# Optimization experiments

Hardware: AMD Instinct MI355X
Metric: run time of the kernel (lower is better)

The kernel has to match this reference:

```python
import jax, jax.numpy as jnp
import numpy as np
from math import sqrt

B, S, E, H = 4, 2048, 1024, 16
DH = E // H  # 64


def setup_inputs() -> dict:
    key = jax.random.key(0)
    ks = jax.random.split(key, 10)
    sc = 0.02
    return {
        "x": jax.random.normal(ks[0], (B, S, E), dtype=jnp.float32),
        # per-head projection weights stacked: [H, E, DH], biases [H, DH]
        "Wq": jax.random.normal(ks[1], (H, E, DH), dtype=jnp.float32) * sc,
        "bq": jax.random.normal(ks[2], (H, DH), dtype=jnp.float32) * sc,
        "Wk": jax.random.normal(ks[3], (H, E, DH), dtype=jnp.float32) * sc,
        "bk": jax.random.normal(ks[4], (H, DH), dtype=jnp.float32) * sc,
        "Wv": jax.random.normal(ks[5], (H, E, DH), dtype=jnp.float32) * sc,
        "bv": jax.random.normal(ks[6], (H, DH), dtype=jnp.float32) * sc,
        "Wo": jax.random.normal(ks[7], (E, E), dtype=jnp.float32) * sc,
        "bo": jax.random.normal(ks[8], (E,), dtype=jnp.float32) * sc,
    }


def reference(x, Wq, bq, Wk, bk, Wv, bv, Wo, bo):
    # Batched QKV projections (equivalent to the per-head Linear loop)
    q = jnp.einsum("bse,hed->bhsd", x, Wq) + bq[None, :, None, :]
    k = jnp.einsum("bse,hed->bhsd", x, Wk) + bk[None, :, None, :]
    v = jnp.einsum("bse,hed->bhsd", x, Wv) + bv[None, :, None, :]
    scores = jnp.einsum("bhsd,bhtd->bhst", q, k) / sqrt(DH)
    # masked=False in the module, so plain softmax over keys
    weights = jax.nn.softmax(scores, axis=-1)
    attn = jnp.einsum("bhst,bhtd->bhsd", weights, v)
    # concat heads: [B,S,H*DH] with head i contiguous (matches torch.cat dim=-1)
    concat = attn.transpose(0, 2, 1, 3).reshape(B, S, H * DH)
    out = concat @ Wo.T if Wo.shape == (E, E) and False else jnp.einsum("bsf,ef->bse", concat, Wo) + bo
    return out
```

## Files before the change

kernel.cpp:

```cpp
#include <hip/hip_runtime.h>
#include <math.h>

#define Bc 4
#define Sc 2048
#define Ec 1024
#define Hc 16
#define DHc 64

typedef unsigned short u16;
typedef __attribute__((ext_vector_type(8))) short short8;
typedef __attribute__((ext_vector_type(4))) float f32x4;
typedef __attribute__((ext_vector_type(16))) float f32x16;
typedef __attribute__((ext_vector_type(2))) unsigned short u16x2;

union pk8 { unsigned int u[4]; short8 v; };

__device__ __forceinline__ u16 f2bf(float f) {
    unsigned int u = __float_as_uint(f);
    u += 0x7FFFu + ((u >> 16) & 1u);
    return (u16)(u >> 16);
}

__device__ __forceinline__ void gl_lds16(const void* g, void* l) {
    __builtin_amdgcn_global_load_lds(
        (const __attribute__((address_space(1))) unsigned int*)g,
        (__attribute__((address_space(3))) unsigned int*)l,
        16, 0, 0);
}

__global__ __launch_bounds__(256)
void prep_kernel(const float* __restrict__ x,
                 const float* __restrict__ Wq, const float* __restrict__ Wk,
                 const float* __restrict__ Wv, const float* __restrict__ Wo,
                 u16* __restrict__ xb, u16* __restrict__ Wob, u16* __restrict__ Wtb)
{
    __shared__ float T[64][65];
    const int bid = blockIdx.x;
    const int t = threadIdx.x;

    if (bid < 4096 + 512) {
        const float* src = (bid < 4096) ? x : Wo;
        u16* dst = (bid < 4096) ? xb : Wob;
        size_t i = (size_t)(bid < 4096 ? bid : bid - 4096) * 256 + t;
        const float* p = src + i * 8;
        float4 a = *(const float4*)p;
        float4 b = *(const float4*)(p + 4);
        short8 v;
        v[0] = (short)f2bf(a.x); v[1] = (short)f2bf(a.y);
        v[2] = (short)f2bf(a.z); v[3] = (short)f2bf(a.w);
        v[4] = (short)f2bf(b.x); v[5] = (short)f2bf(b.y);
        v[6] = (short)f2bf(b.z); v[7] = (short)f2bf(b.w);
        *(short8*)(dst + i * 8) = v;
        return;
    }

    const int bid2 = bid - 4608;
    const int proj = bid2 >> 8;
    const int h = (bid2 >> 4) & 15;
    const int e0 = (bid2 & 15) * 64;
    const float* W = (proj == 0) ? Wq : (proj == 1) ? Wk : Wv;

    #pragma unroll
    for (int i = 0; i < 4; ++i) {
        int fid = t + i * 256;
        int row = fid >> 4, c4 = fid & 15;
        float4 v = *(const float4*)(W + ((size_t)h * Ec + e0 + row) * DHc + c4 * 4);
        T[row][c4 * 4 + 0] = v.x; T[row][c4 * 4 + 1] = v.y;
        T[row][c4 * 4 + 2] = v.z; T[row][c4 * 4 + 3] = v.w;
    }
    __syncthreads();
    const int d = t >> 2, ech = (t & 3) * 16;
    u16* dst = Wtb + ((size_t)(proj * Hc + h) * DHc + d) * Ec + e0 + ech;
    #pragma unroll
    for (int j = 0; j < 16; j += 2) {
        u16x2 v2;
        v2.x = f2bf(T[ech + j][d]);
        v2.y = f2bf(T[ech + j + 1][d]);
        *(u16x2*)(dst + j) = v2;
    }
}

__global__ __launch_bounds__(256)
void qkv_mfma_kernel(const u16* __restrict__ xb, const u16* __restrict__ Wtb,
                     const float* __restrict__ bq, const float* __restrict__ bk,
                     const float* __restrict__ bv,
                     u16* __restrict__ qb, u16* __restrict__ kb, u16* __restrict__ vb)
{
    __shared__ __align__(16) u16 As[128 * 64];
    __shared__ __align__(16) u16 Bs[128 * 64];

    const int t = threadIdx.x;
    const int w = t >> 6, l = t & 63;
    const int wr = w >> 1, wc = w & 1;
    const int mBase = blockIdx.y * 128;
    const int nBase = blockIdx.x * 128;
    const int proj = nBase >> 10;
    const int nIn = nBase & (Ec - 1);
    const int lr = l >> 3, ls = l & 7;
    const int lq = l >> 4, ln = l & 15;

    f32x4 acc[4][4];
    #pragma unroll
    for (int i = 0; i < 4; ++i)
        #pragma unroll
        for (int j = 0; j < 4; ++j) acc[i][j] = (f32x4)0.f;

    for (int k0 = 0; k0 < Ec; k0 += 64) {
        __syncthreads();
        #pragma unroll
        for (int c = 0; c < 8; ++c) {
            int cg = w * 8 + c;
            if (cg < 16) {
                int row = cg * 8 + lr;
                int g = ls ^ (row & 7);
                gl_lds16(xb + ((size_t)(mBase + row)) * Ec + k0 + g * 8,
                         (void*)(As + cg * 512));
            } else {
                int col = (cg - 16) * 8 + lr;
                int g = ls ^ (col & 7);
                gl_lds16(Wtb + ((size_t)proj * Ec + nIn + col) * Ec + k0 + g * 8,
                         (void*)(Bs + (cg - 16) * 512));
            }
        }
        __syncthreads();

        #pragma unroll
        for (int ks = 0; ks < 2; ++ks) {
            short8 af[4], bfr[4];
            int gg = ks * 4 + lq;
            #pragma unroll
            for (int fm = 0; fm < 4; ++fm) {
                int row = wr * 64 + fm * 16 + ln;
                af[fm] = *(const short8*)(As + row * 64 + ((gg ^ (row & 7)) * 8));
            }
            #pragma unroll
            for (int fn = 0; fn < 4; ++fn) {
                int col = wc * 64 + fn * 16 + ln;
                bfr[fn] = *(const short8*)(Bs + col * 64 + ((gg ^ (col & 7)) * 8));
            }
            #pragma unroll
            for (int fm = 0; fm < 4; ++fm)
                #pragma unroll
                for (int fn = 0; fn < 4; ++fn)
                    acc[fm][fn] = __builtin_amdgcn_mfma_f32_16x16x32_bf16(
                        af[fm], bfr[fn], acc[fm][fn], 0, 0, 0);
        }
    }

    const float* bias = (proj == 0) ? bq : (proj == 1) ? bk : bv;
    #pragma unroll
    for (int fn = 0; fn < 4; ++fn) {
        int n = nBase + wc * 64 + fn * 16 + ln;
        int cc = n & (Ec - 1);
        int hh = cc >> 6, d = cc & 63;
        float bv_ = bias[cc];
        #pragma unroll
        for (int fm = 0; fm < 4; ++fm) {
            #pragma unroll
            for (int r = 0; r < 4; ++r) {
                int m = mBase + wr * 64 + fm * 16 + lq * 4 + r;
                int b = m >> 11, s = m & (Sc - 1);
                int bh = b * Hc + hh;
                float vv = acc[fm][fn][r] + bv_;
                if (proj == 0)      qb[((size_t)bh * Sc + s) * DHc + d] = f2bf(vv * 0.18033688011f);
                else if (proj == 1) kb[((size_t)bh * Sc + s) * DHc + d] = f2bf(vv);
                else                vb[((size_t)bh * DHc + d) * Sc + s] = f2bf(vv);
            }
        }
    }
}

__global__ __launch_bounds__(512, 4)
void attn_mfma_kernel(const u16* __restrict__ qb, const u16* __restrict__ kb,
                      const u16* __restrict__ vb, u16* __restrict__ concatb)
{
    __shared__ __align__(16) u16 Kt[2][64 * 64];
    __shared__ __align__(16) u16 Vt[2][64 * 64];

    const int t = threadIdx.x;
    const int w = t >> 6, l = t & 63;
    const int id = blockIdx.x;
    const int j = id >> 3;
    const int qt = j >> 3;
    const int hb = (id & 7) * 8 + (j & 7);
    const int h = hb & 15, b = hb >> 4;
    const int bh = b * Hc + h;
    const int hi = l >> 5, l5 = l & 31;
    const int lr = l >> 3, ls = l & 7;
    const int sw5 = l5 & 7;

    const u16* qp = qb + ((size_t)bh * Sc + qt * 256 + w * 32 + l5) * DHc;
    const u16* kp = kb + (size_t)bh * Sc * DHc;
    const u16* vp = vb + (size_t)bh * DHc * Sc;

    const int cg = w * 2;

    short8 qf[4];
    #pragma unroll
    for (int ks = 0; ks < 4; ++ks)
        qf[ks] = *(const short8*)(qp + ks * 16 + hi * 8);

    f32x16 o0 = (f32x16)0.f, o1 = (f32x16)0.f;
    float m_i = -1e30f, l_i = 0.f;

    #pragma unroll
    for (int c = 0; c < 2; ++c) {
        int g2 = cg + c;
        if (g2 < 8) {
            int row = g2 * 8 + lr;
            int g = ls ^ (row & 7);
            gl_lds16(kp + ((size_t)row) * DHc + g * 8, (void*)(Kt[0] + g2 * 512));
        } else {
            int d = (g2 - 8) * 8 + lr;
            int g = ls ^ (d & 7);
            gl_lds16(vp + (size_t)d * Sc + g * 8, (void*)(Vt[0] + (g2 - 8) * 512));
        }
    }
    asm volatile("s_waitcnt vmcnt(0)" ::: "memory");
    __syncthreads();

    for (int kt = 0; kt < Sc / 64; ++kt) {
        const int cur = kt & 1;
        if (kt + 1 < Sc / 64) {
            const int nxt = cur ^ 1;
            #pragma unroll
            for (int c = 0; c < 2; ++c) {
                int g2 = cg + c;
                if (g2 < 8) {
                    int row = g2 * 8 + lr;
                    int g = ls ^ (row & 7);
                    gl_lds16(kp + ((size_t)((kt + 1) * 64 + row)) * DHc + g * 8,
                             (void*)(Kt[nxt] + g2 * 512));
                } else {
                    int d = (g2 - 8) * 8 + lr;
                    int g = ls ^ (d & 7);
                    gl_lds16(vp + (size_t)d * Sc + (kt + 1) * 64 + g * 8,
                             (void*)(Vt[nxt] + (g2 - 8) * 512));
                }
            }
        }

        f32x16 s0 = (f32x16)0.f, s1 = (f32x16)0.f;
        __builtin_amdgcn_s_setprio(1);
        #pragma unroll
        for (int ks = 0; ks < 4; ++ks) {
            int slot = ((2 * ks + hi) ^ sw5) * 8;
            short8 kf0 = *(const short8*)(Kt[cur] + (l5) * 64 + slot);
            short8 kf1 = *(const short8*)(Kt[cur] + (32 + l5) * 64 + slot);
            s0 = __builtin_amdgcn_mfma_f32_32x32x16_bf16(kf0, qf[ks], s0, 0, 0, 0);
            s1 = __builtin_amdgcn_mfma_f32_32x32x16_bf16(kf1, qf[ks], s1, 0, 0, 0);
        }
        __builtin_amdgcn_s_setprio(0);

        float pm = fmaxf(s0[0], s0[1]);
        #pragma unroll
        for (int r = 2; r < 16; ++r) pm = fmaxf(pm, s0[r]);
        #pragma unroll
        for (int r = 0; r < 16; ++r) pm = fmaxf(pm, s1[r]);
        pm = fmaxf(pm, __shfl_xor(pm, 32));

        bool need = pm > m_i + 8.f;
        if (__any(need)) {
            float nm = fmaxf(m_i, pm);
            float ef = exp2f(m_i - nm);
            l_i *= ef;
            m_i = nm;
            #pragma unroll
            for (int r = 0; r < 16; ++r) {
                int qrow = (r & 3) + 8 * (r >> 2) + 4 * hi;
                float efq = __shfl(ef, qrow);
                o0[r] *= efq; o1[r] *= efq;
            }
        }

        float sum = 0.f;

#define PROC_KG(SV, KG)                                                         \
        {                                                                       \
            float p_[16];                                                       \
            _Pragma("unroll")                                                   \
            for (int r = 0; r < 16; ++r) {                                      \
                p_[r] = exp2f(SV[r] - m_i);                                     \
                sum += p_[r];                                                   \
            }                                                                   \
            unsigned int W_[8];                                                 \
            _Pragma("unroll")                                                   \
            for (int i = 0; i < 8; ++i)                                         \
                asm("v_cvt_pk_bf16_f32 %0, %1, %2"                              \
                    : "=v"(W_[i]) : "v"(p_[2 * i]), "v"(p_[2 * i + 1]));        \
            unsigned int r0 = __shfl_xor(hi ? W_[0] : W_[2], 32);               \
            unsigned int r1 = __shfl_xor(hi ? W_[1] : W_[3], 32);               \
            unsigned int r2 = __shfl_xor(hi ? W_[4] : W_[6], 32);               \
            unsigned int r3 = __shfl_xor(hi ? W_[5] : W_[7], 32);               \
            pk8 a0, a1;                                                         \
            a0.u[0] = hi ? r0 : W_[0];  a0.u[1] = hi ? r1 : W_[1];              \
            a0.u[2] = hi ? W_[2] : r0;  a0.u[3] = hi ? W_[3] : r1;              \
            a1.u[0] = hi ? r2 : W_[4];  a1.u[1] = hi ? r3 : W_[5];              \
            a1.u[2] = hi ? W_[6] : r2;  a1.u[3] = hi ? W_[7] : r3;              \
            _Pragma("unroll")                                                   \
            for (int ksl = 0; ksl < 2; ++ksl) {                                 \
                int slot = (((KG * 4 + ksl * 2 + hi)) ^ sw5) * 8;               \
                short8 vf0 = *(const short8*)(Vt[cur] + (l5) * 64 + slot);      \
                short8 vf1 = *(const short8*)(Vt[cur] + (32 + l5) * 64 + slot); \
                short8 pa = ksl ? a1.v : a0.v;                                  \
                o0 = __builtin_amdgcn_mfma_f32_32x32x16_bf16(pa, vf0, o0, 0, 0, 0); \
                o1 = __builtin_amdgcn_mfma_f32_32x32x16_bf16(pa, vf1, o1, 0, 0, 0); \
            }                                                                   \
        }

        __builtin_amdgcn_s_setprio(1);
        PROC_KG(s0, 0)
        PROC_KG(s1, 1)
        __builtin_amdgcn_s_setprio(0);
#undef PROC_KG

        sum += __shfl_xor(sum, 32);
        l_i += sum;

        asm volatile("s_waitcnt vmcnt(0)" ::: "memory");
        __syncthreads();
    }

    #pragma unroll
    for (int r = 0; r < 16; ++r) {
        int qrow = (r & 3) + 8 * (r >> 2) + 4 * hi;
        float inv = 1.f / __shfl(l_i, qrow);
        int q = qt * 256 + w * 32 + qrow;
        u16* dst = concatb + ((size_t)b * Sc + q) * Ec + h * DHc + l5;
        dst[0]  = f2bf(o0[r] * inv);
        dst[32] = f2bf(o1[r] * inv);
    }
}

__global__ __launch_bounds__(256)
void oproj_mfma_kernel(const u16* __restrict__ cb, const u16* __restrict__ Wob,
                       const float* __restrict__ bo, float* __restrict__ out)
{
    __shared__ __align__(16) u16 As[128 * 64];
    __shared__ __align__(16) u16 Bs[128 * 64];

    const int t = threadIdx.x;
    const int w = t >> 6, l = t & 63;
    const int wr = w >> 1, wc = w & 1;
    const int mBase = blockIdx.y * 128;
    const int nBase = blockIdx.x * 128;
    const int lr = l >> 3, ls = l & 7;
    const int lq = l >> 4, ln = l & 15;

    f32x4 acc[4][4];
    #pragma unroll
    for (int i = 0; i < 4; ++i)
        #pragma unroll
        for (int j = 0; j < 4; ++j) acc[i][j] = (f32x4)0.f;

    for (int k0 = 0; k0 < Ec; k0 += 64) {
        __syncthreads();
        #pragma unroll
        for (int c = 0; c < 8; ++c) {
            int cg = w * 8 + c;
            if (cg < 16) {
                int row = cg * 8 + lr;
                int g = ls ^ (row & 7);
                gl_lds16(cb + ((size_t)(mBase + row)) * Ec + k0 + g * 8,
                         (void*)(As + cg * 512));
            } else {
                int col = (cg - 16) * 8 + lr;
                int g = ls ^ (col & 7);
                gl_lds16(Wob + ((size_t)(nBase + col)) * Ec + k0 + g * 8,
                         (void*)(Bs + (cg - 16) * 512));
            }
        }
        __syncthreads();

        #pragma unroll
        for (int ks = 0; ks < 2; ++ks) {
            short8 af[4], bfr[4];
            int gg = ks * 4 + lq;
            #pragma unroll
            for (int fm = 0; fm < 4; ++fm) {
                int row = wr * 64 + fm * 16 + ln;
                af[fm] = *(const short8*)(As + row * 64 + ((gg ^ (row & 7)) * 8));
            }
            #pragma unroll
            for (int fn = 0; fn < 4; ++fn) {
                int col = wc * 64 + fn * 16 + ln;
                bfr[fn] = *(const short8*)(Bs + col * 64 + ((gg ^ (col & 7)) * 8));
            }
            #pragma unroll
            for (int fm = 0; fm < 4; ++fm)
                #pragma unroll
                for (int fn = 0; fn < 4; ++fn)
                    acc[fm][fn] = __builtin_amdgcn_mfma_f32_16x16x32_bf16(
                        af[fm], bfr[fn], acc[fm][fn], 0, 0, 0);
        }
    }

    #pragma unroll
    for (int fn = 0; fn < 4; ++fn) {
        int n = nBase + wc * 64 + fn * 16 + ln;
        float bb = bo[n];
        #pragma unroll
        for (int fm = 0; fm < 4; ++fm) {
            #pragma unroll
            for (int r = 0; r < 4; ++r) {
                int m = mBase + wr * 64 + fm * 16 + lq * 4 + r;
                out[(size_t)m * Ec + n] = acc[fm][fn][r] + bb;
            }
        }
    }
}

extern "C" void kernel_launch(void* const* d_in, const int* in_sizes, int n_in,
                              void* d_out, int out_size, void* d_ws, size_t ws_size,
                              hipStream_t stream)
{
    const float* x  = (const float*)d_in[0];
    const float* Wq = (const float*)d_in[1];
    const float* bq = (const float*)d_in[2];
    const float* Wk = (const float*)d_in[3];
    const float* bk = (const float*)d_in[4];
    const float* Wv = (const float*)d_in[5];
    const float* bv = (const float*)d_in[6];
    const float* Wo = (const float*)d_in[7];
    const float* bo = (const float*)d_in[8];
    float* out = (float*)d_out;

    char* ws = (char*)d_ws;
    u16* xb   = (u16*)(ws);
    u16* Wtb  = (u16*)(ws + (16u << 20));
    u16* Wob  = (u16*)(ws + (22u << 20));
    u16* qbuf = (u16*)(ws + (24u << 20));
    u16* kbuf = (u16*)(ws + (40u << 20));
    u16* vbuf = (u16*)(ws + (56u << 20));
    u16* cbuf = (u16*)(ws + (72u << 20));

    prep_kernel<<<dim3(5376, 1, 1), 256, 0, stream>>>(x, Wq, Wk, Wv, Wo, xb, Wob, Wtb);

    dim3 g1(3 * Ec / 128, (Bc * Sc) / 128);
    qkv_mfma_kernel<<<g1, 256, 0, stream>>>(xb, Wtb, bq, bk, bv, qbuf, kbuf, vbuf);

    attn_mfma_kernel<<<dim3(512, 1, 1), 512, 0, stream>>>(qbuf, kbuf, vbuf, cbuf);

    dim3 g3(Ec / 128, (Bc * Sc) / 128);
    oproj_mfma_kernel<<<g3, 256, 0, stream>>>(cbuf, Wob, bo, out);
}
```

Baseline: 235.4 us.

## Double-buffer QKV and output-projection GEMMs with larger tiles and swizzled grid

Both projection GEMMs move from 128x128 tiles with 4 waves to 128x256 tiles with 8 waves. The A and B LDS buffers are now double-buffered, so global-to-LDS loads for the next K tile are issued while MFMAs run on the current one, and wave priority is raised during the MFMA bursts. Each K tile is split into two halves to interleave the loads. Block IDs are remapped so neighbouring blocks share M tiles, which should help L2 reuse. The cost is more LDS per block (96 KB) and more barriers per K tile, which can limit occupancy.

New measurement: 255.3 us. +8.5%, slower.

```diff
diff --git a/kernel.cpp b/kernel.cpp
--- a/kernel.cpp
+++ b/kernel.cpp
@@ -80,20 +80,22 @@
     }
 }
 
-__global__ __launch_bounds__(256)
+__global__ __launch_bounds__(512, 2)
 void qkv_mfma_kernel(const u16* __restrict__ xb, const u16* __restrict__ Wtb,
                      const float* __restrict__ bq, const float* __restrict__ bk,
                      const float* __restrict__ bv,
                      u16* __restrict__ qb, u16* __restrict__ kb, u16* __restrict__ vb)
 {
-    __shared__ __align__(16) u16 As[128 * 64];
-    __shared__ __align__(16) u16 Bs[128 * 64];
+    __shared__ __align__(16) u16 As[2][128 * 64];
+    __shared__ __align__(16) u16 Bs[2][256 * 64];
 
     const int t = threadIdx.x;
     const int w = t >> 6, l = t & 63;
-    const int wr = w >> 1, wc = w & 1;
-    const int mBase = blockIdx.y * 128;
-    const int nBase = blockIdx.x * 128;
+    const int wr = w >> 2, wc = w & 3;
+    const int id = blockIdx.x;
+    const int j = id >> 3;
+    const int mBase = ((id & 7) * 8 + (j & 7)) * 128;
+    const int nBase = (j >> 3) * 256;
     const int proj = nBase >> 10;
     const int nIn = nBase & (Ec - 1);
     const int lr = l >> 3, ls = l & 7;
@@ -103,49 +105,57 @@
     #pragma unroll
     for (int i = 0; i < 4; ++i)
         #pragma unroll
-        for (int j = 0; j < 4; ++j) acc[i][j] = (f32x4)0.f;
-
-    for (int k0 = 0; k0 < Ec; k0 += 64) {
-        __syncthreads();
-        #pragma unroll
-        for (int c = 0; c < 8; ++c) {
-            int cg = w * 8 + c;
-            if (cg < 16) {
-                int row = cg * 8 + lr;
-                int g = ls ^ (row & 7);
-                gl_lds16(xb + ((size_t)(mBase + row)) * Ec + k0 + g * 8,
-                         (void*)(As + cg * 512));
-            } else {
-                int col = (cg - 16) * 8 + lr;
-                int g = ls ^ (col & 7);
-                gl_lds16(Wtb + ((size_t)proj * Ec + nIn + col) * Ec + k0 + g * 8,
-                         (void*)(Bs + (cg - 16) * 512));
-            }
-        }
-        __syncthreads();
-
-        #pragma unroll
-        for (int ks = 0; ks < 2; ++ks) {
-            short8 af[4], bfr[4];
-            int gg = ks * 4 + lq;
-            #pragma unroll
-            for (int fm = 0; fm < 4; ++fm) {
-                int row = wr * 64 + fm * 16 + ln;
-                af[fm] = *(const short8*)(As + row * 64 + ((gg ^ (row & 7)) * 8));
-            }
-            #pragma unroll
-            for (int fn = 0; fn < 4; ++fn) {
-                int col = wc * 64 + fn * 16 + ln;
-                bfr[fn] = *(const short8*)(Bs + col * 64 + ((gg ^ (col & 7)) * 8));
-            }
-            #pragma unroll
-            for (int fm = 0; fm < 4; ++fm)
+        for (int jj = 0; jj < 4; ++jj) acc[i][jj] = (f32x4)0.f;
+
+    #define STAGE_QKV(CH, KT, BUF)                                              \
+        { int ch_ = (CH);                                                       \
+          if (ch_ < 16) { int R = ch_ * 8 + lr; int g = ls ^ (R & 7);           \
+              gl_lds16(xb + ((size_t)(mBase + R)) * Ec + (KT) * 64 + g * 8,     \
+                       (void*)(As[BUF] + ch_ * 512)); }                         \
+          else { int C2 = (ch_ - 16) * 8 + lr; int g = ls ^ (C2 & 7);           \
+              gl_lds16(Wtb + ((size_t)proj * Ec + nIn + C2) * Ec + (KT) * 64 + g * 8, \
+                       (void*)(Bs[BUF] + (ch_ - 16) * 512)); } }
+
+    #pragma unroll
+    for (int c = 0; c < 6; ++c) STAGE_QKV(w * 6 + c, 0, 0)
+    asm volatile("s_waitcnt vmcnt(0)" ::: "memory");
+    __builtin_amdgcn_s_barrier();
+
+    for (int kt = 0; kt < 16; ++kt) {
+        const int cb = kt & 1;
+        #pragma unroll
+        for (int p = 0; p < 2; ++p) {
+            if (kt + 1 < 16) {
                 #pragma unroll
-                for (int fn = 0; fn < 4; ++fn)
-                    acc[fm][fn] = __builtin_amdgcn_mfma_f32_16x16x32_bf16(
-                        af[fm], bfr[fn], acc[fm][fn], 0, 0, 0);
-        }
-    }
+                for (int c = 0; c < 3; ++c) STAGE_QKV(w * 6 + p * 3 + c, kt + 1, cb ^ 1)
+            }
+            short8 af[4], bf8[4];
+            int gg = p * 4 + lq;
+            #pragma unroll
+            for (int i = 0; i < 4; ++i) {
+                int row = wr * 64 + i * 16 + ln;
+                af[i] = *(const short8*)(As[cb] + row * 64 + ((gg ^ (row & 7)) * 8));
+            }
+            #pragma unroll
+            for (int i = 0; i < 4; ++i) {
+                int col = wc * 64 + i * 16 + ln;
+                bf8[i] = *(const short8*)(Bs[cb] + col * 64 + ((gg ^ (col & 7)) * 8));
+            }
+            __builtin_amdgcn_s_barrier();
+            asm volatile("s_waitcnt lgkmcnt(0)" ::: "memory");
+            __builtin_amdgcn_s_setprio(1);
+            #pragma unroll
+            for (int i = 0; i < 4; ++i)
+                #pragma unroll
+                for (int n2 = 0; n2 < 4; ++n2)
+                    acc[i][n2] = __builtin_amdgcn_mfma_f32_16x16x32_bf16(
+                        af[i], bf8[n2], acc[i][n2], 0, 0, 0);
+            __builtin_amdgcn_s_setprio(0);
+            if (p == 1) asm volatile("s_waitcnt vmcnt(0)" ::: "memory");
+            __builtin_amdgcn_s_barrier();
+        }
+    }
+    #undef STAGE_QKV
 
     const float* bias = (proj == 0) ? bq : (proj == 1) ? bk : bv;
     #pragma unroll
@@ -332,18 +342,20 @@
     }
 }
 
-__global__ __launch_bounds__(256)
-void oproj_mfma_kernel(const u16* __restrict__ cb, const u16* __restrict__ Wob,
+__global__ __launch_bounds__(512, 2)
+void oproj_mfma_kernel(const u16* __restrict__ cb2, const u16* __restrict__ Wob,
                        const float* __restrict__ bo, float* __restrict__ out)
 {
-    __shared__ __align__(16) u16 As[128 * 64];
-    __shared__ __align__(16) u16 Bs[128 * 64];
+    __shared__ __align__(16) u16 As[2][128 * 64];
+    __shared__ __align__(16) u16 Bs[2][256 * 64];
 
     const int t = threadIdx.x;
     const int w = t >> 6, l = t & 63;
-    const int wr = w >> 1, wc = w & 1;
-    const int mBase = blockIdx.y * 128;
-    const int nBase = blockIdx.x * 128;
+    const int wr = w >> 2, wc = w & 3;
+    const int id = blockIdx.x;
+    const int j = id >> 3;
+    const int mBase = ((id & 7) * 8 + (j & 7)) * 128;
+    const int nBase = (j >> 3) * 256;
     const int lr = l >> 3, ls = l & 7;
     const int lq = l >> 4, ln = l & 15;
 
@@ -351,49 +363,57 @@
     #pragma unroll
     for (int i = 0; i < 4; ++i)
         #pragma unroll
-        for (int j = 0; j < 4; ++j) acc[i][j] = (f32x4)0.f;
-
-    for (int k0 = 0; k0 < Ec; k0 += 64) {
-        __syncthreads();
-        #pragma unroll
-        for (int c = 0; c < 8; ++c) {
-            int cg = w * 8 + c;
-            if (cg < 16) {
-                int row = cg * 8 + lr;
-                int g = ls ^ (row & 7);
-                gl_lds16(cb + ((size_t)(mBase + row)) * Ec + k0 + g * 8,
-                         (void*)(As + cg * 512));
-            } else {
-                int col = (cg - 16) * 8 + lr;
-                int g = ls ^ (col & 7);
-                gl_lds16(Wob + ((size_t)(nBase + col)) * Ec + k0 + g * 8,
-                         (void*)(Bs + (cg - 16) * 512));
-            }
-        }
-        __syncthreads();
-
-        #pragma unroll
-        for (int ks = 0; ks < 2; ++ks) {
-            short8 af[4], bfr[4];
-            int gg = ks * 4 + lq;
-            #pragma unroll
-            for (int fm = 0; fm < 4; ++fm) {
-                int row = wr * 64 + fm * 16 + ln;
-                af[fm] = *(const short8*)(As + row * 64 + ((gg ^ (row & 7)) * 8));
-            }
-            #pragma unroll
-            for (int fn = 0; fn < 4; ++fn) {
-                int col = wc * 64 + fn * 16 + ln;
-                bfr[fn] = *(const short8*)(Bs + col * 64 + ((gg ^ (col & 7)) * 8));
-            }
-            #pragma unroll
-            for (int fm = 0; fm < 4; ++fm)
+        for (int jj = 0; jj < 4; ++jj) acc[i][jj] = (f32x4)0.f;
+
+    #define STAGE_OP(CH, KT, BUF)                                               \
+        { int ch_ = (CH);                                                       \
+          if (ch_ < 16) { int R = ch_ * 8 + lr; int g = ls ^ (R & 7);           \
+              gl_lds16(cb2 + ((size_t)(mBase + R)) * Ec + (KT) * 64 + g * 8,    \
+                       (void*)(As[BUF] + ch_ * 512)); }                         \
+          else { int C2 = (ch_ - 16) * 8 + lr; int g = ls ^ (C2 & 7);           \
+              gl_lds16(Wob + ((size_t)(nBase + C2)) * Ec + (KT) * 64 + g * 8,   \
+                       (void*)(Bs[BUF] + (ch_ - 16) * 512)); } }
+
+    #pragma unroll
+    for (int c = 0; c < 6; ++c) STAGE_OP(w * 6 + c, 0, 0)
+    asm volatile("s_waitcnt vmcnt(0)" ::: "memory");
+    __builtin_amdgcn_s_barrier();
+
+    for (int kt = 0; kt < 16; ++kt) {
+        const int cbuf = kt & 1;
+        #pragma unroll
+        for (int p = 0; p < 2; ++p) {
+            if (kt + 1 < 16) {
                 #pragma unroll
-                for (int fn = 0; fn < 4; ++fn)
-                    acc[fm][fn] = __builtin_amdgcn_mfma_f32_16x16x32_bf16(
-                        af[fm], bfr[fn], acc[fm][fn], 0, 0, 0);
-        }
-    }
+                for (int c = 0; c < 3; ++c) STAGE_OP(w * 6 + p * 3 + c, kt + 1, cbuf ^ 1)
+            }
+            short8 af[4], bf8[4];
+            int gg = p * 4 + lq;
+            #pragma unroll
+            for (int i = 0; i < 4; ++i) {
+                int row = wr * 64 + i * 16 + ln;
+                af[i] = *(const short8*)(As[cbuf] + row * 64 + ((gg ^ (row & 7)) * 8));
+            }
+            #pragma unroll
+            for (int i = 0; i < 4; ++i) {
+                int col = wc * 64 + i * 16 + ln;
+                bf8[i] = *(const short8*)(Bs[cbuf] + col * 64 + ((gg ^ (col & 7)) * 8));
+            }
+            __builtin_amdgcn_s_barrier();
+            asm volatile("s_waitcnt lgkmcnt(0)" ::: "memory");
+            __builtin_amdgcn_s_setprio(1);
+            #pragma unroll
+            for (int i = 0; i < 4; ++i)
+                #pragma unroll
+                for (int n2 = 0; n2 < 4; ++n2)
+                    acc[i][n2] = __builtin_amdgcn_mfma_f32_16x16x32_bf16(
+                        af[i], bf8[n2], acc[i][n2], 0, 0, 0);
+            __builtin_amdgcn_s_setprio(0);
+            if (p == 1) asm volatile("s_waitcnt vmcnt(0)" ::: "memory");
+            __builtin_amdgcn_s_barrier();
+        }
+    }
+    #undef STAGE_OP
 
     #pragma unroll
     for (int fn = 0; fn < 4; ++fn) {
@@ -436,11 +456,9 @@
 
     prep_kernel<<<dim3(5376, 1, 1), 256, 0, stream>>>(x, Wq, Wk, Wv, Wo, xb, Wob, Wtb);
 
-    dim3 g1(3 * Ec / 128, (Bc * Sc) / 128);
-    qkv_mfma_kernel<<<g1, 256, 0, stream>>>(xb, Wtb, bq, bk, bv, qbuf, kbuf, vbuf);
+    qkv_mfma_kernel<<<dim3(768, 1, 1), 512, 0, stream>>>(xb, Wtb, bq, bk, bv, qbuf, kbuf, vbuf);
 
     attn_mfma_kernel<<<dim3(512, 1, 1), 512, 0, stream>>>(qbuf, kbuf, vbuf, cbuf);
 
-    dim3 g3(Ec / 128, (Bc * Sc) / 128);
-    oproj_mfma_kernel<<<g3, 256, 0, stream>>>(cbuf, Wob, bo, out);
-}
+    oproj_mfma_kernel<<<dim3(256, 1, 1), 512, 0, stream>>>(cbuf, Wob, bo, out);
+}
```
